# Kernel optimization log

Measured on AMD Instinct MI355X. Metric: run time of the kernel, lower is better.

The kernel has to match this reference:

```python
import jax, jax.numpy as jnp
import numpy as np

B, S, H, E, I_E, V = 4, 4096, 1024, 8, 512, 100000


def setup_inputs() -> dict:
    key = jax.random.key(0)
    k0, k1, k2, k3, k4, k5, k6 = jax.random.split(key, 7)
    hidden_states = jax.random.normal(k0, (B, S, H), dtype=jnp.float32)
    token_ids = jax.random.randint(k1, (B, S), 0, V, dtype=jnp.int64)
    mu = jax.random.normal(k2, (B, S, H), dtype=jnp.float32)
    # torch Linear(in,out,bias=False) weight is [out,in]; we store transposed [in,out]
    w_gate = jax.random.normal(k3, (E, H, I_E), dtype=jnp.float32) * 0.02
    w_up = jax.random.normal(k4, (E, H, I_E), dtype=jnp.float32) * 0.02
    w_down = jax.random.normal(k5, (E, I_E, H), dtype=jnp.float32) * 0.02
    # module zero-inits mu_router; use small random so the mu-override path is exercised
    mu_router_w = jax.random.normal(k6, (E, H), dtype=jnp.float32) * 0.02
    return {
        "hidden_states": hidden_states,
        "token_ids": token_ids,
        "mu": mu,
        "w_gate": w_gate,
        "w_up": w_up,
        "w_down": w_down,
        "mu_router_w": mu_router_w,
    }


def reference(hidden_states, token_ids, mu, w_gate, w_up, w_down, mu_router_w):
    num_experts = w_gate.shape[0]
    # deterministic token->expert mapping: token_id % num_experts (after clamp)
    tid = jnp.clip(token_ids, 0, V - 1)
    base_expert_ids = (tid % num_experts).astype(jnp.int32)  # [B,S]
    # mu-guided override: one_hot*10 + mu_logits, argmax
    mu_logits = jnp.einsum("bsh,eh->bse", mu, mu_router_w)
    base_one_hot = jax.nn.one_hot(base_expert_ids, num_experts, dtype=mu_logits.dtype)
    expert_ids = jnp.argmax(base_one_hot * 10.0 + mu_logits, axis=-1)  # [B,S]

    x = hidden_states.reshape(-1, H)          # [T,H], T=B*S
    eid = expert_ids.reshape(-1)              # [T]
    out = jnp.zeros_like(x)
    for e in range(num_experts):
        mask = (eid == e)[:, None]            # [T,1]
        g = x @ w_gate[e]                     # [T,I_E]
        u = x @ w_up[e]                       # [T,I_E]
        y = (jax.nn.silu(g) * u) @ w_down[e]  # [T,H] SwiGLU
        out = out + jnp.where(mask, y, 0.0)
    return out.reshape(hidden_states.shape)
```

## Files before the change

kernel.cpp:

```cpp
#include <hip/hip_runtime.h>
#include <stdint.h>

#define T_TOK   16384
#define H_DIM   1024
#define IE_DIM  512
#define E_NUM   8
#define V_MAX   100000

typedef __attribute__((ext_vector_type(8))) short bf16x8;
typedef __attribute__((ext_vector_type(4))) float f32x4;
typedef unsigned long long ull;

__device__ __forceinline__ unsigned short f2bf(float f) {
  union { float f; unsigned u; } v; v.f = f;
  unsigned r = v.u + 0x7fffu + ((v.u >> 16) & 1u);
  return (unsigned short)(r >> 16);
}

__device__ __forceinline__ void gload16(const void* g, void* l) {
  __builtin_amdgcn_global_load_lds(
      (const __attribute__((address_space(1))) unsigned int*)g,
      (__attribute__((address_space(3))) unsigned int*)(unsigned int)(uintptr_t)l,
      16, 0, 0);
}

__global__ __launch_bounds__(256) void k_pre(
    const float* __restrict__ mu, const int* __restrict__ tok,
    const float* __restrict__ mrw, int* __restrict__ eid,
    int* __restrict__ blockCnt,
    const float* __restrict__ wg, const float* __restrict__ wu,
    const float* __restrict__ wd, unsigned short* __restrict__ WgT,
    unsigned short* __restrict__ WuT, unsigned short* __restrict__ WdT) {
  __shared__ unsigned short lds[64][72];
  int tid = threadIdx.x;

  if (blockIdx.x < 1024) {
    int* cnt = (int*)&lds[0][0];
    if (tid < 8) cnt[tid] = 0;
    int wv = blockIdx.x * 4 + (tid >> 6);
    int t0 = wv * 4;
    int lane = tid & 63;
    const float4* mrw4 = (const float4*)mrw;

    float acc[4][E_NUM];
#pragma unroll
    for (int i = 0; i < 4; i++)
#pragma unroll
      for (int e = 0; e < E_NUM; e++) acc[i][e] = 0.f;

#pragma unroll
    for (int j = 0; j < 4; j++) {
      int idx = lane + 64 * j;
      float4 wr[E_NUM];
#pragma unroll
      for (int e = 0; e < E_NUM; e++) wr[e] = mrw4[e * 256 + idx];
#pragma unroll
      for (int i = 0; i < 4; i++) {
        float4 m = ((const float4*)(mu + (size_t)(t0 + i) * H_DIM))[idx];
#pragma unroll
        for (int e = 0; e < E_NUM; e++)
          acc[i][e] += m.x * wr[e].x + m.y * wr[e].y + m.z * wr[e].z + m.w * wr[e].w;
      }
    }
#pragma unroll
    for (int i = 0; i < 4; i++)
#pragma unroll
      for (int e = 0; e < E_NUM; e++)
#pragma unroll
        for (int off = 32; off >= 1; off >>= 1)
          acc[i][e] += __shfl_xor(acc[i][e], off, 64);

    __syncthreads();
#pragma unroll
    for (int i = 0; i < 4; i++) {
      int tv = tok[t0 + i];
      if (tv < 0) tv = 0;
      if (tv > V_MAX - 1) tv = V_MAX - 1;
      int base = tv & 7;
      int best = 0; float bs = -1e30f;
#pragma unroll
      for (int e = 0; e < E_NUM; e++) {
        float s = acc[i][e] + (e == base ? 10.f : 0.f);
        if (s > bs) { bs = s; best = e; }
      }
      if (lane == i) {
        eid[t0 + i] = best;
        atomicAdd(&cnt[best], 1);
      }
    }
    __syncthreads();
    if (tid < 8) blockCnt[blockIdx.x * 8 + tid] = cnt[tid];
  } else {
    int sel = (blockIdx.x - 1024) >> 10;
    int blk = blockIdx.x & 1023;
    const float* src; unsigned short* dst; int R, C;
    if (sel == 0)      { src = wg; dst = WgT; R = H_DIM; C = IE_DIM; }
    else if (sel == 1) { src = wu; dst = WuT; R = H_DIM; C = IE_DIM; }
    else               { src = wd; dst = WdT; R = IE_DIM; C = H_DIM; }
    int tpe = (R >> 6) * (C >> 6);
    int e = blk / tpe;
    int rem = blk % tpe;
    int tr = rem / (C >> 6);
    int tc = rem % (C >> 6);
    const float* s = src + (size_t)e * R * C;
    unsigned short* d = dst + (size_t)e * R * C;
    int r0 = tid >> 4;
    int c0 = (tid & 15) * 4;
#pragma unroll
    for (int i = 0; i < 4; i++) {
      int r = r0 + i * 16;
      float4 v = *(const float4*)(s + (size_t)(tr * 64 + r) * C + tc * 64 + c0);
      lds[r][c0 + 0] = f2bf(v.x); lds[r][c0 + 1] = f2bf(v.y);
      lds[r][c0 + 2] = f2bf(v.z); lds[r][c0 + 3] = f2bf(v.w);
    }
    __syncthreads();
    int oc = tid >> 2;
    int ob = (tid & 3) * 16;
    unsigned short tmp[16];
#pragma unroll
    for (int i = 0; i < 16; i++) tmp[i] = lds[ob + i][oc];
    uint4* dp = (uint4*)(d + (size_t)(tc * 64 + oc) * R + tr * 64 + ob);
    dp[0] = ((uint4*)tmp)[0];
    dp[1] = ((uint4*)tmp)[1];
  }
}

__global__ __launch_bounds__(1024) void k_scan2(
    const int* __restrict__ blockCnt, int* __restrict__ blockBase,
    int* __restrict__ offsets, int* __restrict__ tileOff) {
  int b = threadIdx.x;
  __shared__ ull s0[1024], s1[1024];
  __shared__ int offL[8];
  const int4* p = (const int4*)(blockCnt + b * 8);
  int4 x0 = p[0], x1 = p[1];
  int c[8] = {x0.x, x0.y, x0.z, x0.w, x1.x, x1.y, x1.z, x1.w};
  ull v0 = (ull)c[0] | ((ull)c[1] << 16) | ((ull)c[2] << 32) | ((ull)c[3] << 48);
  ull v1 = (ull)c[4] | ((ull)c[5] << 16) | ((ull)c[6] << 32) | ((ull)c[7] << 48);
  s0[b] = v0; s1[b] = v1;
  __syncthreads();
  for (int st = 1; st < 1024; st <<= 1) {
    ull a0 = 0, a1 = 0;
    if (b >= st) { a0 = s0[b - st]; a1 = s1[b - st]; }
    __syncthreads();
    v0 += a0; v1 += a1;
    s0[b] = v0; s1[b] = v1;
    __syncthreads();
  }
  if (b == 1023) {
    int tot[8];
#pragma unroll
    for (int e = 0; e < 4; e++) tot[e] = (int)((v0 >> (16 * e)) & 0xFFFF);
#pragma unroll
    for (int e = 0; e < 4; e++) tot[4 + e] = (int)((v1 >> (16 * e)) & 0xFFFF);
    int s = 0, ts = 0;
    for (int e = 0; e < E_NUM; e++) {
      offsets[e] = s; offL[e] = s; tileOff[e] = ts;
      s += tot[e];
      ts += (tot[e] + 127) >> 7;
    }
    offsets[E_NUM] = s; tileOff[E_NUM] = ts;
  }
  __syncthreads();
  int be[8];
#pragma unroll
  for (int e = 0; e < 4; e++)
    be[e] = offL[e] + (int)((v0 >> (16 * e)) & 0xFFFF) - c[e];
#pragma unroll
  for (int e = 0; e < 4; e++)
    be[4 + e] = offL[4 + e] + (int)((v1 >> (16 * e)) & 0xFFFF) - c[4 + e];
  int4* q = (int4*)(blockBase + b * 8);
  q[0] = make_int4(be[0], be[1], be[2], be[3]);
  q[1] = make_int4(be[4], be[5], be[6], be[7]);
}

__global__ __launch_bounds__(256) void k_gather(
    const float* __restrict__ hs, const int* __restrict__ eid,
    const int* __restrict__ blockBase, int* __restrict__ tokofrow,
    unsigned short* __restrict__ Xs) {
  int b = blockIdx.x;
  int tid = threadIdx.x;
  __shared__ int eL[16];
  __shared__ int posL[16];
  if (tid < 16) eL[tid] = eid[b * 16 + tid];
  __syncthreads();
  if (tid < 16) {
    int e = eL[tid];
    int r = 0;
    for (int j = 0; j < tid; j++) r += (eL[j] == e);
    int pos = blockBase[b * 8 + e] + r;
    posL[tid] = pos;
    tokofrow[pos] = b * 16 + tid;
  }
  __syncthreads();
  int w = tid >> 6, lane = tid & 63;
#pragma unroll
  for (int i = 0; i < 4; i++) {
    int li = w * 4 + i;
    int t = b * 16 + li;
    int pos = posL[li];
    const float4* src = (const float4*)(hs + (size_t)t * H_DIM);
    unsigned short* drow = Xs + (size_t)pos * H_DIM;
#pragma unroll
    for (int j = 0; j < 4; j++) {
      float4 v = src[lane + 64 * j];
      ushort4 bb;
      bb.x = f2bf(v.x); bb.y = f2bf(v.y); bb.z = f2bf(v.z); bb.w = f2bf(v.w);
      *(ushort4*)(drow + (lane + 64 * j) * 4) = bb;
    }
  }
}

__global__ __launch_bounds__(256, 2) void k_gemm1(
    const unsigned short* __restrict__ Xs,
    const unsigned short* __restrict__ WgT,
    const unsigned short* __restrict__ WuT,
    unsigned short* __restrict__ Hb,
    const int* __restrict__ offsets, const int* __restrict__ tileOff) {
  int nt = blockIdx.x & 3;
  int mlin = blockIdx.x >> 2;
  if (mlin >= tileOff[E_NUM]) return;
  int e = 0;
#pragma unroll
  for (int i = 1; i < E_NUM; i++)
    if (mlin >= tileOff[i]) e = i;
  int mtile = mlin - tileOff[e];
  int segStart = offsets[e], segEnd = offsets[e + 1];
  int M = segEnd - segStart;

  __shared__ unsigned short Alds[3][128 * 32];
  __shared__ unsigned short Bglds[3][128 * 32];
  __shared__ unsigned short Bulds[3][128 * 32];

  int tid = threadIdx.x;
  int lane = tid & 63;
  int w = tid >> 6;
  int wm = w >> 1;
  int wn = w & 1;

  f32x4 accg[4][4], accu[4][4];
#pragma unroll
  for (int i = 0; i < 4; i++)
#pragma unroll
    for (int j = 0; j < 4; j++) {
      accg[i][j] = (f32x4)(0.f);
      accu[i][j] = (f32x4)(0.f);
    }

  int sr = tid >> 2;
  int sc = tid & 3;
  int scc = sc ^ ((sr >> 1) & 3);
  int g0 = mtile * 128 + sr;       if (g0 > M - 1) g0 = M - 1;
  int g1 = mtile * 128 + 64 + sr;  if (g1 > M - 1) g1 = M - 1;
  const unsigned short* A0 = Xs + (size_t)(segStart + g0) * H_DIM + scc * 8;
  const unsigned short* A1 = Xs + (size_t)(segStart + g1) * H_DIM + scc * 8;
  const unsigned short* Bgb = WgT + (size_t)e * IE_DIM * H_DIM;
  const unsigned short* Bub = WuT + (size_t)e * IE_DIM * H_DIM;
  const unsigned short* Bg0 = Bgb + (size_t)(nt * 128 + sr) * H_DIM + scc * 8;
  const unsigned short* Bg1 = Bgb + (size_t)(nt * 128 + 64 + sr) * H_DIM + scc * 8;
  const unsigned short* Bu0 = Bub + (size_t)(nt * 128 + sr) * H_DIM + scc * 8;
  const unsigned short* Bu1 = Bub + (size_t)(nt * 128 + 64 + sr) * H_DIM + scc * 8;

#define STAGE1(buf, k0)                                               \
  {                                                                   \
    gload16(A0 + (k0), (char*)Alds[buf] + tid * 16);                  \
    gload16(A1 + (k0), (char*)Alds[buf] + 4096 + tid * 16);           \
    gload16(Bg0 + (k0), (char*)Bglds[buf] + tid * 16);                \
    gload16(Bg1 + (k0), (char*)Bglds[buf] + 4096 + tid * 16);         \
    gload16(Bu0 + (k0), (char*)Bulds[buf] + tid * 16);                \
    gload16(Bu1 + (k0), (char*)Bulds[buf] + 4096 + tid * 16);         \
  }

  int kc = lane >> 4;
  int abyte[4], bbyte[4];
#pragma unroll
  for (int f = 0; f < 4; f++) {
    int ra = wm * 64 + f * 16 + (lane & 15);
    abyte[f] = ra * 64 + ((kc ^ ((ra >> 1) & 3)) << 4);
    int rb = wn * 64 + f * 16 + (lane & 15);
    bbyte[f] = rb * 64 + ((kc ^ ((rb >> 1) & 3)) << 4);
  }

  const int NT = H_DIM / 32;
  STAGE1(0, 0);
  STAGE1(1, 32);

  int cur = 0;
  for (int t = 0; t < NT; t++) {
    asm volatile("s_waitcnt vmcnt(6)" ::: "memory");
    __builtin_amdgcn_s_barrier();
    __builtin_amdgcn_sched_barrier(0);
    int tn = t + 2; if (tn >= NT) tn -= NT;
    int nbuf = cur + 2; if (nbuf >= 3) nbuf -= 3;
    STAGE1(nbuf, tn * 32);

    bf16x8 a[4], bg[4], bu[4];
#pragma unroll
    for (int f = 0; f < 4; f++) {
      a[f]  = *(const bf16x8*)((const char*)Alds[cur] + abyte[f]);
      bg[f] = *(const bf16x8*)((const char*)Bglds[cur] + bbyte[f]);
      bu[f] = *(const bf16x8*)((const char*)Bulds[cur] + bbyte[f]);
    }
#pragma unroll
    for (int mf = 0; mf < 4; mf++)
#pragma unroll
      for (int nf = 0; nf < 4; nf++) {
        accg[mf][nf] = __builtin_amdgcn_mfma_f32_16x16x32_bf16(
            a[mf], bg[nf], accg[mf][nf], 0, 0, 0);
        accu[mf][nf] = __builtin_amdgcn_mfma_f32_16x16x32_bf16(
            a[mf], bu[nf], accu[mf][nf], 0, 0, 0);
      }
    cur = (cur + 1 == 3) ? 0 : cur + 1;
  }
#undef STAGE1
  asm volatile("s_waitcnt vmcnt(0)" ::: "memory");

  int rowBase = segStart + mtile * 128 + wm * 64;
#pragma unroll
  for (int mf = 0; mf < 4; mf++)
#pragma unroll
    for (int nf = 0; nf < 4; nf++) {
      int col = nt * 128 + wn * 64 + nf * 16 + (lane & 15);
#pragma unroll
      for (int j = 0; j < 4; j++) {
        int r = rowBase + mf * 16 + (lane >> 4) * 4 + j;
        if (r < segEnd) {
          float g = accg[mf][nf][j];
          float u = accu[mf][nf][j];
          float h = (g / (1.f + __expf(-g))) * u;
          Hb[(size_t)r * IE_DIM + col] = f2bf(h);
        }
      }
    }
}

__global__ __launch_bounds__(256, 4) void k_gemm2(
    const unsigned short* __restrict__ Hb,
    const unsigned short* __restrict__ WdT,
    float* __restrict__ out,
    const int* __restrict__ offsets, const int* __restrict__ tileOff,
    const int* __restrict__ tokofrow) {
  int nt = blockIdx.x & 7;
  int mlin = blockIdx.x >> 3;
  if (mlin >= tileOff[E_NUM]) return;
  int e = 0;
#pragma unroll
  for (int i = 1; i < E_NUM; i++)
    if (mlin >= tileOff[i]) e = i;
  int mtile = mlin - tileOff[e];
  int segStart = offsets[e], segEnd = offsets[e + 1];
  int M = segEnd - segStart;

  __shared__ unsigned short Alds[3][128 * 32];
  __shared__ unsigned short Blds[3][128 * 32];

  int tid = threadIdx.x;
  int lane = tid & 63;
  int w = tid >> 6;
  int wm = w >> 1;
  int wn = w & 1;

  f32x4 acc[4][4];
#pragma unroll
  for (int i = 0; i < 4; i++)
#pragma unroll
    for (int j = 0; j < 4; j++) acc[i][j] = (f32x4)(0.f);

  int sr = tid >> 2;
  int sc = tid & 3;
  int scc = sc ^ ((sr >> 1) & 3);
  int g0 = mtile * 128 + sr;       if (g0 > M - 1) g0 = M - 1;
  int g1 = mtile * 128 + 64 + sr;  if (g1 > M - 1) g1 = M - 1;
  const unsigned short* A0 = Hb + (size_t)(segStart + g0) * IE_DIM + scc * 8;
  const unsigned short* A1 = Hb + (size_t)(segStart + g1) * IE_DIM + scc * 8;
  const unsigned short* Bb = WdT + (size_t)e * H_DIM * IE_DIM;
  const unsigned short* B0 = Bb + (size_t)(nt * 128 + sr) * IE_DIM + scc * 8;
  const unsigned short* B1 = Bb + (size_t)(nt * 128 + 64 + sr) * IE_DIM + scc * 8;

#define STAGE2(buf, k0)                                              \
  {                                                                  \
    gload16(A0 + (k0), (char*)Alds[buf] + tid * 16);                 \
    gload16(A1 + (k0), (char*)Alds[buf] + 4096 + tid * 16);          \
    gload16(B0 + (k0), (char*)Blds[buf] + tid * 16);                 \
    gload16(B1 + (k0), (char*)Blds[buf] + 4096 + tid * 16);          \
  }

  int kc = lane >> 4;
  int abyte[4], bbyte[4];
#pragma unroll
  for (int f = 0; f < 4; f++) {
    int ra = wm * 64 + f * 16 + (lane & 15);
    abyte[f] = ra * 64 + ((kc ^ ((ra >> 1) & 3)) << 4);
    int rb = wn * 64 + f * 16 + (lane & 15);
    bbyte[f] = rb * 64 + ((kc ^ ((rb >> 1) & 3)) << 4);
  }

  const int NT = IE_DIM / 32;
  STAGE2(0, 0);
  STAGE2(1, 32);

  int cur = 0;
  for (int t = 0; t < NT; t++) {
    asm volatile("s_waitcnt vmcnt(4)" ::: "memory");
    __builtin_amdgcn_s_barrier();
    __builtin_amdgcn_sched_barrier(0);
    int tn = t + 2; if (tn >= NT) tn -= NT;
    int nbuf = cur + 2; if (nbuf >= 3) nbuf -= 3;
    STAGE2(nbuf, tn * 32);

    bf16x8 a[4], b[4];
#pragma unroll
    for (int f = 0; f < 4; f++) {
      a[f] = *(const bf16x8*)((const char*)Alds[cur] + abyte[f]);
      b[f] = *(const bf16x8*)((const char*)Blds[cur] + bbyte[f]);
    }
#pragma unroll
    for (int mf = 0; mf < 4; mf++)
#pragma unroll
      for (int nf = 0; nf < 4; nf++)
        acc[mf][nf] = __builtin_amdgcn_mfma_f32_16x16x32_bf16(
            a[mf], b[nf], acc[mf][nf], 0, 0, 0);
    cur = (cur + 1 == 3) ? 0 : cur + 1;
  }
#undef STAGE2
  asm volatile("s_waitcnt vmcnt(0)" ::: "memory");

  int rowBase = segStart + mtile * 128 + wm * 64;
#pragma unroll
  for (int mf = 0; mf < 4; mf++)
#pragma unroll
    for (int nf = 0; nf < 4; nf++) {
      int col = nt * 128 + wn * 64 + nf * 16 + (lane & 15);
#pragma unroll
      for (int j = 0; j < 4; j++) {
        int r = rowBase + mf * 16 + (lane >> 4) * 4 + j;
        if (r < segEnd) {
          int t = tokofrow[r];
          out[(size_t)t * H_DIM + col] = acc[mf][nf][j];
        }
      }
    }
}

#define WS_XS    ((size_t)0)
#define WS_WGT   ((size_t)33554432)
#define WS_WUT   ((size_t)41943040)
#define WS_WDT   ((size_t)50331648)
#define WS_HB    ((size_t)58720256)
#define WS_EID   ((size_t)75497472)
#define WS_TOK   ((size_t)75563008)
#define WS_OFF   ((size_t)75628544)
#define WS_BC    ((size_t)75629568)
#define WS_BB    ((size_t)75662336)

extern "C" void kernel_launch(void* const* d_in, const int* in_sizes, int n_in,
                              void* d_out, int out_size, void* d_ws, size_t ws_size,
                              hipStream_t stream) {
  const float* hs  = (const float*)d_in[0];
  const int*   tok = (const int*)d_in[1];
  const float* mu  = (const float*)d_in[2];
  const float* wg  = (const float*)d_in[3];
  const float* wu  = (const float*)d_in[4];
  const float* wd  = (const float*)d_in[5];
  const float* mrw = (const float*)d_in[6];
  float* out = (float*)d_out;
  char* ws = (char*)d_ws;

  unsigned short* Xs  = (unsigned short*)(ws + WS_XS);
  unsigned short* WgT = (unsigned short*)(ws + WS_WGT);
  unsigned short* WuT = (unsigned short*)(ws + WS_WUT);
  unsigned short* WdT = (unsigned short*)(ws + WS_WDT);
  unsigned short* Hb  = (unsigned short*)(ws + WS_HB);
  int* eid      = (int*)(ws + WS_EID);
  int* tokofrow = (int*)(ws + WS_TOK);
  int* offsets  = (int*)(ws + WS_OFF);
  int* tileOff  = offsets + 16;
  int* blockCnt = (int*)(ws + WS_BC);
  int* blockBase= (int*)(ws + WS_BB);

  k_pre<<<4096, 256, 0, stream>>>(mu, tok, mrw, eid, blockCnt,
                                  wg, wu, wd, WgT, WuT, WdT);
  k_scan2<<<1, 1024, 0, stream>>>(blockCnt, blockBase, offsets, tileOff);
  k_gather<<<1024, 256, 0, stream>>>(hs, eid, blockBase, tokofrow, Xs);
  k_gemm1<<<135 * 4, 256, 0, stream>>>(Xs, WgT, WuT, Hb, offsets, tileOff);
  k_gemm2<<<135 * 8, 256, 0, stream>>>(Hb, WdT, out, offsets, tileOff, tokofrow);
}
```

Measured before the change: 172.1 us.

## Halve gemm1 N-tile, remap block IDs across XCDs, raise MFMA priority

gemm1 now uses a 128x64 output tile per gate/up matrix instead of 128x128, which doubles the grid to 1080 blocks and halves accumulator registers and B-tile LDS so three blocks fit per CU. Both GEMMs remap blockIdx with a stride-135 permutation so that consecutive hardware block IDs, which are spread across XCDs, land on tiles sharing weights or rows. s_setprio is raised around the MFMA loops. Occupancy for gemm2 drops from 4 to 3. The narrower gemm1 tile re-reads the A operand twice as often.

```diff
diff --git a/kernel.cpp b/kernel.cpp
--- a/kernel.cpp
+++ b/kernel.cpp
@@ -210,14 +210,16 @@
   }
 }
 
-__global__ __launch_bounds__(256, 2) void k_gemm1(
+__global__ __launch_bounds__(256, 3) void k_gemm1(
     const unsigned short* __restrict__ Xs,
     const unsigned short* __restrict__ WgT,
     const unsigned short* __restrict__ WuT,
     unsigned short* __restrict__ Hb,
     const int* __restrict__ offsets, const int* __restrict__ tileOff) {
-  int nt = blockIdx.x & 3;
-  int mlin = blockIdx.x >> 2;
+  int bid0 = blockIdx.x;
+  int wg = (bid0 & 7) * 135 + (bid0 >> 3);
+  int nt = wg & 7;
+  int mlin = wg >> 3;
   if (mlin >= tileOff[E_NUM]) return;
   int e = 0;
 #pragma unroll
@@ -228,8 +230,8 @@
   int M = segEnd - segStart;
 
   __shared__ unsigned short Alds[3][128 * 32];
-  __shared__ unsigned short Bglds[3][128 * 32];
-  __shared__ unsigned short Bulds[3][128 * 32];
+  __shared__ unsigned short Bglds[3][64 * 32];
+  __shared__ unsigned short Bulds[3][64 * 32];
 
   int tid = threadIdx.x;
   int lane = tid & 63;
@@ -237,47 +239,49 @@
   int wm = w >> 1;
   int wn = w & 1;
 
-  f32x4 accg[4][4], accu[4][4];
+  f32x4 accg[4][2], accu[4][2];
 #pragma unroll
   for (int i = 0; i < 4; i++)
 #pragma unroll
-    for (int j = 0; j < 4; j++) {
+    for (int j = 0; j < 2; j++) {
       accg[i][j] = (f32x4)(0.f);
       accu[i][j] = (f32x4)(0.f);
     }
 
-  int sr = tid >> 2;
-  int sc = tid & 3;
-  int scc = sc ^ ((sr >> 1) & 3);
-  int g0 = mtile * 128 + sr;       if (g0 > M - 1) g0 = M - 1;
-  int g1 = mtile * 128 + 64 + sr;  if (g1 > M - 1) g1 = M - 1;
-  const unsigned short* A0 = Xs + (size_t)(segStart + g0) * H_DIM + scc * 8;
-  const unsigned short* A1 = Xs + (size_t)(segStart + g1) * H_DIM + scc * 8;
-  const unsigned short* Bgb = WgT + (size_t)e * IE_DIM * H_DIM;
-  const unsigned short* Bub = WuT + (size_t)e * IE_DIM * H_DIM;
-  const unsigned short* Bg0 = Bgb + (size_t)(nt * 128 + sr) * H_DIM + scc * 8;
-  const unsigned short* Bg1 = Bgb + (size_t)(nt * 128 + 64 + sr) * H_DIM + scc * 8;
-  const unsigned short* Bu0 = Bub + (size_t)(nt * 128 + sr) * H_DIM + scc * 8;
-  const unsigned short* Bu1 = Bub + (size_t)(nt * 128 + 64 + sr) * H_DIM + scc * 8;
+  int ar0 = tid >> 2, ac0 = tid & 3;
+  int ar1 = (tid + 256) >> 2, ac1 = tid & 3;
+  int acc0 = ac0 ^ ((ar0 >> 1) & 3);
+  int acc1 = ac1 ^ ((ar1 >> 1) & 3);
+  int g0 = mtile * 128 + ar0; if (g0 > M - 1) g0 = M - 1;
+  int g1 = mtile * 128 + ar1; if (g1 > M - 1) g1 = M - 1;
+  const unsigned short* A0 = Xs + (size_t)(segStart + g0) * H_DIM + acc0 * 8;
+  const unsigned short* A1 = Xs + (size_t)(segStart + g1) * H_DIM + acc1 * 8;
+  int br = tid >> 2, bc = tid & 3;
+  int bcc = bc ^ ((br >> 1) & 3);
+  const unsigned short* Bg0 =
+      WgT + (size_t)e * IE_DIM * H_DIM + (size_t)(nt * 64 + br) * H_DIM + bcc * 8;
+  const unsigned short* Bu0 =
+      WuT + (size_t)e * IE_DIM * H_DIM + (size_t)(nt * 64 + br) * H_DIM + bcc * 8;
 
 #define STAGE1(buf, k0)                                               \
   {                                                                   \
     gload16(A0 + (k0), (char*)Alds[buf] + tid * 16);                  \
     gload16(A1 + (k0), (char*)Alds[buf] + 4096 + tid * 16);           \
     gload16(Bg0 + (k0), (char*)Bglds[buf] + tid * 16);                \
-    gload16(Bg1 + (k0), (char*)Bglds[buf] + 4096 + tid * 16);         \
     gload16(Bu0 + (k0), (char*)Bulds[buf] + tid * 16);                \
-    gload16(Bu1 + (k0), (char*)Bulds[buf] + 4096 + tid * 16);         \
   }
 
   int kc = lane >> 4;
-  int abyte[4], bbyte[4];
-#pragma unroll
-  for (int f = 0; f < 4; f++) {
-    int ra = wm * 64 + f * 16 + (lane & 15);
-    abyte[f] = ra * 64 + ((kc ^ ((ra >> 1) & 3)) << 4);
-    int rb = wn * 64 + f * 16 + (lane & 15);
-    bbyte[f] = rb * 64 + ((kc ^ ((rb >> 1) & 3)) << 4);
+  int abyte[4], bbyte[2];
+#pragma unroll
+  for (int mf = 0; mf < 4; mf++) {
+    int row = wm * 64 + mf * 16 + (lane & 15);
+    abyte[mf] = row * 64 + ((kc ^ ((row >> 1) & 3)) << 4);
+  }
+#pragma unroll
+  for (int nf = 0; nf < 2; nf++) {
+    int row = wn * 32 + nf * 16 + (lane & 15);
+    bbyte[nf] = row * 64 + ((kc ^ ((row >> 1) & 3)) << 4);
   }
 
   const int NT = H_DIM / 32;
@@ -286,29 +290,33 @@
 
   int cur = 0;
   for (int t = 0; t < NT; t++) {
-    asm volatile("s_waitcnt vmcnt(6)" ::: "memory");
+    asm volatile("s_waitcnt vmcnt(4)" ::: "memory");
     __builtin_amdgcn_s_barrier();
     __builtin_amdgcn_sched_barrier(0);
     int tn = t + 2; if (tn >= NT) tn -= NT;
     int nbuf = cur + 2; if (nbuf >= 3) nbuf -= 3;
     STAGE1(nbuf, tn * 32);
 
-    bf16x8 a[4], bg[4], bu[4];
-#pragma unroll
-    for (int f = 0; f < 4; f++) {
-      a[f]  = *(const bf16x8*)((const char*)Alds[cur] + abyte[f]);
-      bg[f] = *(const bf16x8*)((const char*)Bglds[cur] + bbyte[f]);
-      bu[f] = *(const bf16x8*)((const char*)Bulds[cur] + bbyte[f]);
-    }
+    bf16x8 a[4], bg[2], bu[2];
 #pragma unroll
     for (int mf = 0; mf < 4; mf++)
-#pragma unroll
-      for (int nf = 0; nf < 4; nf++) {
+      a[mf] = *(const bf16x8*)((const char*)Alds[cur] + abyte[mf]);
+#pragma unroll
+    for (int nf = 0; nf < 2; nf++) {
+      bg[nf] = *(const bf16x8*)((const char*)Bglds[cur] + bbyte[nf]);
+      bu[nf] = *(const bf16x8*)((const char*)Bulds[cur] + bbyte[nf]);
+    }
+    __builtin_amdgcn_s_setprio(1);
+#pragma unroll
+    for (int mf = 0; mf < 4; mf++)
+#pragma unroll
+      for (int nf = 0; nf < 2; nf++) {
         accg[mf][nf] = __builtin_amdgcn_mfma_f32_16x16x32_bf16(
             a[mf], bg[nf], accg[mf][nf], 0, 0, 0);
         accu[mf][nf] = __builtin_amdgcn_mfma_f32_16x16x32_bf16(
             a[mf], bu[nf], accu[mf][nf], 0, 0, 0);
       }
+    __builtin_amdgcn_s_setprio(0);
     cur = (cur + 1 == 3) ? 0 : cur + 1;
   }
 #undef STAGE1
@@ -318,8 +326,8 @@
 #pragma unroll
   for (int mf = 0; mf < 4; mf++)
 #pragma unroll
-    for (int nf = 0; nf < 4; nf++) {
-      int col = nt * 128 + wn * 64 + nf * 16 + (lane & 15);
+    for (int nf = 0; nf < 2; nf++) {
+      int col = nt * 64 + wn * 32 + nf * 16 + (lane & 15);
 #pragma unroll
       for (int j = 0; j < 4; j++) {
         int r = rowBase + mf * 16 + (lane >> 4) * 4 + j;
@@ -333,14 +341,16 @@
     }
 }
 
-__global__ __launch_bounds__(256, 4) void k_gemm2(
+__global__ __launch_bounds__(256, 3) void k_gemm2(
     const unsigned short* __restrict__ Hb,
     const unsigned short* __restrict__ WdT,
     float* __restrict__ out,
     const int* __restrict__ offsets, const int* __restrict__ tileOff,
     const int* __restrict__ tokofrow) {
-  int nt = blockIdx.x & 7;
-  int mlin = blockIdx.x >> 3;
+  int bid0 = blockIdx.x;
+  int wg = (bid0 & 7) * 135 + (bid0 >> 3);
+  int nt = wg & 7;
+  int mlin = wg >> 3;
   if (mlin >= tileOff[E_NUM]) return;
   int e = 0;
 #pragma unroll
@@ -365,16 +375,17 @@
 #pragma unroll
     for (int j = 0; j < 4; j++) acc[i][j] = (f32x4)(0.f);
 
-  int sr = tid >> 2;
-  int sc = tid & 3;
-  int scc = sc ^ ((sr >> 1) & 3);
-  int g0 = mtile * 128 + sr;       if (g0 > M - 1) g0 = M - 1;
-  int g1 = mtile * 128 + 64 + sr;  if (g1 > M - 1) g1 = M - 1;
-  const unsigned short* A0 = Hb + (size_t)(segStart + g0) * IE_DIM + scc * 8;
-  const unsigned short* A1 = Hb + (size_t)(segStart + g1) * IE_DIM + scc * 8;
+  int ar0 = tid >> 2, ac0 = tid & 3;
+  int ar1 = (tid + 256) >> 2;
+  int acc0 = ac0 ^ ((ar0 >> 1) & 3);
+  int acc1 = ac0 ^ ((ar1 >> 1) & 3);
+  int g0 = mtile * 128 + ar0; if (g0 > M - 1) g0 = M - 1;
+  int g1 = mtile * 128 + ar1; if (g1 > M - 1) g1 = M - 1;
+  const unsigned short* A0 = Hb + (size_t)(segStart + g0) * IE_DIM + acc0 * 8;
+  const unsigned short* A1 = Hb + (size_t)(segStart + g1) * IE_DIM + acc1 * 8;
   const unsigned short* Bb = WdT + (size_t)e * H_DIM * IE_DIM;
-  const unsigned short* B0 = Bb + (size_t)(nt * 128 + sr) * IE_DIM + scc * 8;
-  const unsigned short* B1 = Bb + (size_t)(nt * 128 + 64 + sr) * IE_DIM + scc * 8;
+  const unsigned short* B0 = Bb + (size_t)(nt * 128 + ar0) * IE_DIM + acc0 * 8;
+  const unsigned short* B1 = Bb + (size_t)(nt * 128 + ar1) * IE_DIM + acc1 * 8;
 
 #define STAGE2(buf, k0)                                              \
   {                                                                  \
@@ -413,12 +424,14 @@
       a[f] = *(const bf16x8*)((const char*)Alds[cur] + abyte[f]);
       b[f] = *(const bf16x8*)((const char*)Blds[cur] + bbyte[f]);
     }
+    __builtin_amdgcn_s_setprio(1);
 #pragma unroll
     for (int mf = 0; mf < 4; mf++)
 #pragma unroll
       for (int nf = 0; nf < 4; nf++)
         acc[mf][nf] = __builtin_amdgcn_mfma_f32_16x16x32_bf16(
             a[mf], b[nf], acc[mf][nf], 0, 0, 0);
+    __builtin_amdgcn_s_setprio(0);
     cur = (cur + 1 == 3) ? 0 : cur + 1;
   }
 #undef STAGE2
@@ -481,6 +494,6 @@
                                   wg, wu, wd, WgT, WuT, WdT);
   k_scan2<<<1, 1024, 0, stream>>>(blockCnt, blockBase, offsets, tileOff);
   k_gather<<<1024, 256, 0, stream>>>(hs, eid, blockBase, tokofrow, Xs);
-  k_gemm1<<<135 * 4, 256, 0, stream>>>(Xs, WgT, WuT, Hb, offsets, tileOff);
+  k_gemm1<<<135 * 8, 256, 0, stream>>>(Xs, WgT, WuT, Hb, offsets, tileOff);
   k_gemm2<<<135 * 8, 256, 0, stream>>>(Hb, WdT, out, offsets, tileOff, tokofrow);
 }
```

New measurement: 158.4 us. 1.09x faster.

## Enlarge MoE GEMM tiles to 256 rows with 512-thread blocks and XCD remap

Applied to the files above, without the earlier changes.

Both expert GEMMs move from 128-row to 256-row M tiles using 512-thread workgroups. gemm2 also widens N tiles to 256 columns. The goal is to raise operand reuse per LDS load and cut the number of tiles. Block IDs are remapped so consecutive workgroups stay on the same XCD for better L2 sharing, and MFMA sections are wrapped in s_setprio. Larger tiles mean more padding waste on partially filled expert segments, fewer blocks (284) to fill the CUs, and higher LDS and register pressure, including 128 accumulator vectors per thread in gemm2.

```diff
diff --git a/kernel.cpp b/kernel.cpp
--- a/kernel.cpp
+++ b/kernel.cpp
@@ -156,7 +156,7 @@
     for (int e = 0; e < E_NUM; e++) {
       offsets[e] = s; offL[e] = s; tileOff[e] = ts;
       s += tot[e];
-      ts += (tot[e] + 127) >> 7;
+      ts += (tot[e] + 255) >> 8;
     }
     offsets[E_NUM] = s; tileOff[E_NUM] = ts;
   }
@@ -210,14 +210,17 @@
   }
 }
 
-__global__ __launch_bounds__(256, 2) void k_gemm1(
+__global__ __launch_bounds__(512, 2) void k_gemm1(
     const unsigned short* __restrict__ Xs,
     const unsigned short* __restrict__ WgT,
     const unsigned short* __restrict__ WuT,
     unsigned short* __restrict__ Hb,
     const int* __restrict__ offsets, const int* __restrict__ tileOff) {
-  int nt = blockIdx.x & 3;
-  int mlin = blockIdx.x >> 2;
+  int bid0 = blockIdx.x;
+  int xcd = bid0 & 7, seq = bid0 >> 3;
+  int wg = (xcd < 4 ? xcd * 36 : 144 + (xcd - 4) * 35) + seq;
+  int nt = wg & 3;
+  int mlin = wg >> 2;
   if (mlin >= tileOff[E_NUM]) return;
   int e = 0;
 #pragma unroll
@@ -227,7 +230,7 @@
   int segStart = offsets[e], segEnd = offsets[e + 1];
   int M = segEnd - segStart;
 
-  __shared__ unsigned short Alds[3][128 * 32];
+  __shared__ unsigned short Alds[3][256 * 32];
   __shared__ unsigned short Bglds[3][128 * 32];
   __shared__ unsigned short Bulds[3][128 * 32];
 
@@ -246,28 +249,26 @@
       accu[i][j] = (f32x4)(0.f);
     }
 
-  int sr = tid >> 2;
-  int sc = tid & 3;
-  int scc = sc ^ ((sr >> 1) & 3);
-  int g0 = mtile * 128 + sr;       if (g0 > M - 1) g0 = M - 1;
-  int g1 = mtile * 128 + 64 + sr;  if (g1 > M - 1) g1 = M - 1;
-  const unsigned short* A0 = Xs + (size_t)(segStart + g0) * H_DIM + scc * 8;
-  const unsigned short* A1 = Xs + (size_t)(segStart + g1) * H_DIM + scc * 8;
-  const unsigned short* Bgb = WgT + (size_t)e * IE_DIM * H_DIM;
-  const unsigned short* Bub = WuT + (size_t)e * IE_DIM * H_DIM;
-  const unsigned short* Bg0 = Bgb + (size_t)(nt * 128 + sr) * H_DIM + scc * 8;
-  const unsigned short* Bg1 = Bgb + (size_t)(nt * 128 + 64 + sr) * H_DIM + scc * 8;
-  const unsigned short* Bu0 = Bub + (size_t)(nt * 128 + sr) * H_DIM + scc * 8;
-  const unsigned short* Bu1 = Bub + (size_t)(nt * 128 + 64 + sr) * H_DIM + scc * 8;
+  int ar0 = tid >> 2, ac = tid & 3;
+  int ar1 = ar0 + 128;
+  int acs = ac ^ ((ar0 >> 1) & 3);
+  int g0 = mtile * 256 + ar0; if (g0 > M - 1) g0 = M - 1;
+  int g1 = mtile * 256 + ar1; if (g1 > M - 1) g1 = M - 1;
+  const unsigned short* A0 = Xs + (size_t)(segStart + g0) * H_DIM + acs * 8;
+  const unsigned short* A1 = Xs + (size_t)(segStart + g1) * H_DIM + acs * 8;
+  int br = tid >> 2;
+  int bcs = (tid & 3) ^ ((br >> 1) & 3);
+  const unsigned short* Bg0 =
+      WgT + (size_t)e * IE_DIM * H_DIM + (size_t)(nt * 128 + br) * H_DIM + bcs * 8;
+  const unsigned short* Bu0 =
+      WuT + (size_t)e * IE_DIM * H_DIM + (size_t)(nt * 128 + br) * H_DIM + bcs * 8;
 
 #define STAGE1(buf, k0)                                               \
   {                                                                   \
     gload16(A0 + (k0), (char*)Alds[buf] + tid * 16);                  \
-    gload16(A1 + (k0), (char*)Alds[buf] + 4096 + tid * 16);           \
+    gload16(A1 + (k0), (char*)Alds[buf] + 8192 + tid * 16);           \
     gload16(Bg0 + (k0), (char*)Bglds[buf] + tid * 16);                \
-    gload16(Bg1 + (k0), (char*)Bglds[buf] + 4096 + tid * 16);         \
     gload16(Bu0 + (k0), (char*)Bulds[buf] + tid * 16);                \
-    gload16(Bu1 + (k0), (char*)Bulds[buf] + 4096 + tid * 16);         \
   }
 
   int kc = lane >> 4;
@@ -286,7 +287,7 @@
 
   int cur = 0;
   for (int t = 0; t < NT; t++) {
-    asm volatile("s_waitcnt vmcnt(6)" ::: "memory");
+    asm volatile("s_waitcnt vmcnt(4)" ::: "memory");
     __builtin_amdgcn_s_barrier();
     __builtin_amdgcn_sched_barrier(0);
     int tn = t + 2; if (tn >= NT) tn -= NT;
@@ -300,6 +301,7 @@
       bg[f] = *(const bf16x8*)((const char*)Bglds[cur] + bbyte[f]);
       bu[f] = *(const bf16x8*)((const char*)Bulds[cur] + bbyte[f]);
     }
+    __builtin_amdgcn_s_setprio(1);
 #pragma unroll
     for (int mf = 0; mf < 4; mf++)
 #pragma unroll
@@ -309,12 +311,13 @@
         accu[mf][nf] = __builtin_amdgcn_mfma_f32_16x16x32_bf16(
             a[mf], bu[nf], accu[mf][nf], 0, 0, 0);
       }
+    __builtin_amdgcn_s_setprio(0);
     cur = (cur + 1 == 3) ? 0 : cur + 1;
   }
 #undef STAGE1
   asm volatile("s_waitcnt vmcnt(0)" ::: "memory");
 
-  int rowBase = segStart + mtile * 128 + wm * 64;
+  int rowBase = segStart + mtile * 256 + wm * 64;
 #pragma unroll
   for (int mf = 0; mf < 4; mf++)
 #pragma unroll
@@ -333,14 +336,17 @@
     }
 }
 
-__global__ __launch_bounds__(256, 4) void k_gemm2(
+__global__ __launch_bounds__(512, 2) void k_gemm2(
     const unsigned short* __restrict__ Hb,
     const unsigned short* __restrict__ WdT,
     float* __restrict__ out,
     const int* __restrict__ offsets, const int* __restrict__ tileOff,
     const int* __restrict__ tokofrow) {
-  int nt = blockIdx.x & 7;
-  int mlin = blockIdx.x >> 3;
+  int bid0 = blockIdx.x;
+  int xcd = bid0 & 7, seq = bid0 >> 3;
+  int wg = (xcd < 4 ? xcd * 36 : 144 + (xcd - 4) * 35) + seq;
+  int nt = wg & 3;
+  int mlin = wg >> 2;
   if (mlin >= tileOff[E_NUM]) return;
   int e = 0;
 #pragma unroll
@@ -350,8 +356,8 @@
   int segStart = offsets[e], segEnd = offsets[e + 1];
   int M = segEnd - segStart;
 
-  __shared__ unsigned short Alds[3][128 * 32];
-  __shared__ unsigned short Blds[3][128 * 32];
+  __shared__ unsigned short Alds[3][256 * 32];
+  __shared__ unsigned short Blds[3][256 * 32];
 
   int tid = threadIdx.x;
   int lane = tid & 63;
@@ -359,38 +365,41 @@
   int wm = w >> 1;
   int wn = w & 1;
 
-  f32x4 acc[4][4];
+  f32x4 acc[4][8];
 #pragma unroll
   for (int i = 0; i < 4; i++)
 #pragma unroll
-    for (int j = 0; j < 4; j++) acc[i][j] = (f32x4)(0.f);
-
-  int sr = tid >> 2;
-  int sc = tid & 3;
-  int scc = sc ^ ((sr >> 1) & 3);
-  int g0 = mtile * 128 + sr;       if (g0 > M - 1) g0 = M - 1;
-  int g1 = mtile * 128 + 64 + sr;  if (g1 > M - 1) g1 = M - 1;
-  const unsigned short* A0 = Hb + (size_t)(segStart + g0) * IE_DIM + scc * 8;
-  const unsigned short* A1 = Hb + (size_t)(segStart + g1) * IE_DIM + scc * 8;
+    for (int j = 0; j < 8; j++) acc[i][j] = (f32x4)(0.f);
+
+  int ar0 = tid >> 2, ac = tid & 3;
+  int ar1 = ar0 + 128;
+  int acs = ac ^ ((ar0 >> 1) & 3);
+  int g0 = mtile * 256 + ar0; if (g0 > M - 1) g0 = M - 1;
+  int g1 = mtile * 256 + ar1; if (g1 > M - 1) g1 = M - 1;
+  const unsigned short* A0 = Hb + (size_t)(segStart + g0) * IE_DIM + acs * 8;
+  const unsigned short* A1 = Hb + (size_t)(segStart + g1) * IE_DIM + acs * 8;
   const unsigned short* Bb = WdT + (size_t)e * H_DIM * IE_DIM;
-  const unsigned short* B0 = Bb + (size_t)(nt * 128 + sr) * IE_DIM + scc * 8;
-  const unsigned short* B1 = Bb + (size_t)(nt * 128 + 64 + sr) * IE_DIM + scc * 8;
+  const unsigned short* B0 = Bb + (size_t)(nt * 256 + ar0) * IE_DIM + acs * 8;
+  const unsigned short* B1 = Bb + (size_t)(nt * 256 + ar1) * IE_DIM + acs * 8;
 
 #define STAGE2(buf, k0)                                              \
   {                                                                  \
     gload16(A0 + (k0), (char*)Alds[buf] + tid * 16);                 \
-    gload16(A1 + (k0), (char*)Alds[buf] + 4096 + tid * 16);          \
+    gload16(A1 + (k0), (char*)Alds[buf] + 8192 + tid * 16);          \
     gload16(B0 + (k0), (char*)Blds[buf] + tid * 16);                 \
-    gload16(B1 + (k0), (char*)Blds[buf] + 4096 + tid * 16);          \
+    gload16(B1 + (k0), (char*)Blds[buf] + 8192 + tid * 16);          \
   }
 
   int kc = lane >> 4;
-  int abyte[4], bbyte[4];
+  int abyte[4], bbyte[8];
 #pragma unroll
   for (int f = 0; f < 4; f++) {
     int ra = wm * 64 + f * 16 + (lane & 15);
     abyte[f] = ra * 64 + ((kc ^ ((ra >> 1) & 3)) << 4);
-    int rb = wn * 64 + f * 16 + (lane & 15);
+  }
+#pragma unroll
+  for (int f = 0; f < 8; f++) {
+    int rb = wn * 128 + f * 16 + (lane & 15);
     bbyte[f] = rb * 64 + ((kc ^ ((rb >> 1) & 3)) << 4);
   }
 
@@ -407,29 +416,32 @@
     int nbuf = cur + 2; if (nbuf >= 3) nbuf -= 3;
     STAGE2(nbuf, tn * 32);
 
-    bf16x8 a[4], b[4];
-#pragma unroll
-    for (int f = 0; f < 4; f++) {
+    bf16x8 a[4], b[8];
+#pragma unroll
+    for (int f = 0; f < 4; f++)
       a[f] = *(const bf16x8*)((const char*)Alds[cur] + abyte[f]);
+#pragma unroll
+    for (int f = 0; f < 8; f++)
       b[f] = *(const bf16x8*)((const char*)Blds[cur] + bbyte[f]);
-    }
+    __builtin_amdgcn_s_setprio(1);
 #pragma unroll
     for (int mf = 0; mf < 4; mf++)
 #pragma unroll
-      for (int nf = 0; nf < 4; nf++)
+      for (int nf = 0; nf < 8; nf++)
         acc[mf][nf] = __builtin_amdgcn_mfma_f32_16x16x32_bf16(
             a[mf], b[nf], acc[mf][nf], 0, 0, 0);
+    __builtin_amdgcn_s_setprio(0);
     cur = (cur + 1 == 3) ? 0 : cur + 1;
   }
 #undef STAGE2
   asm volatile("s_waitcnt vmcnt(0)" ::: "memory");
 
-  int rowBase = segStart + mtile * 128 + wm * 64;
+  int rowBase = segStart + mtile * 256 + wm * 64;
 #pragma unroll
   for (int mf = 0; mf < 4; mf++)
 #pragma unroll
-    for (int nf = 0; nf < 4; nf++) {
-      int col = nt * 128 + wn * 64 + nf * 16 + (lane & 15);
+    for (int nf = 0; nf < 8; nf++) {
+      int col = nt * 256 + wn * 128 + nf * 16 + (lane & 15);
 #pragma unroll
       for (int j = 0; j < 4; j++) {
         int r = rowBase + mf * 16 + (lane >> 4) * 4 + j;
@@ -481,6 +493,6 @@
                                   wg, wu, wd, WgT, WuT, WdT);
   k_scan2<<<1, 1024, 0, stream>>>(blockCnt, blockBase, offsets, tileOff);
   k_gather<<<1024, 256, 0, stream>>>(hs, eid, blockBase, tokofrow, Xs);
-  k_gemm1<<<135 * 4, 256, 0, stream>>>(Xs, WgT, WuT, Hb, offsets, tileOff);
-  k_gemm2<<<135 * 8, 256, 0, stream>>>(Hb, WdT, out, offsets, tileOff, tokofrow);
-}
+  k_gemm1<<<284, 512, 0, stream>>>(Xs, WgT, WuT, Hb, offsets, tileOff);
+  k_gemm2<<<284, 512, 0, stream>>>(Hb, WdT, out, offsets, tileOff, tokofrow);
+}
```

After: 191.8 us. +11.4%, slower.
